# Kernel optimization log

Measured on AMD Instinct MI355X. Metric: run time of the kernel, lower is better.

The kernel has to match this reference:

```python
import jax, jax.numpy as jnp
import numpy as np

N_EMBD = 768
N_HEAD = 12
HEAD_DIM = N_EMBD // N_HEAD


def setup_inputs() -> dict:
    key = jax.random.key(0)
    k0, k1, k2, k3, k4 = jax.random.split(key, 5)
    B, T, C = 2, 4096, N_EMBD
    x = jax.random.normal(k0, (B, T, C), dtype=jnp.float32)
    # c_attn: Linear(C, 3C); c_proj: Linear(C, C). torch Linear: y = x @ W.T + b
    s = 1.0 / np.sqrt(C)
    W_attn = jax.random.uniform(k1, (3 * C, C), dtype=jnp.float32, minval=-s, maxval=s)
    b_attn = jax.random.uniform(k2, (3 * C,), dtype=jnp.float32, minval=-s, maxval=s)
    W_proj = jax.random.uniform(k3, (C, C), dtype=jnp.float32, minval=-s, maxval=s)
    b_proj = jax.random.uniform(k4, (C,), dtype=jnp.float32, minval=-s, maxval=s)
    return {"x": x, "W_attn": W_attn, "b_attn": b_attn, "W_proj": W_proj, "b_proj": b_proj}


def reference(x, W_attn, b_attn, W_proj, b_proj):
    B, T, C = x.shape
    H, D = N_HEAD, HEAD_DIM
    qkv = x @ W_attn.T + b_attn                      # [B,T,3C]
    q, k, v = jnp.split(qkv, 3, axis=-1)
    # [B,T,C] -> [B,H,T,D]
    q = q.reshape(B, T, H, D).transpose(0, 2, 1, 3)
    k = k.reshape(B, T, H, D).transpose(0, 2, 1, 3)
    v = v.reshape(B, T, H, D).transpose(0, 2, 1, 3)
    scale = 1.0 / jnp.sqrt(jnp.asarray(D, dtype=x.dtype))
    att = jnp.einsum('bhqd,bhkd->bhqk', q, k) * scale  # [B,H,T,T]
    att = jax.nn.softmax(att, axis=-1)
    y = jnp.einsum('bhqk,bhkd->bhqd', att, v)          # [B,H,T,D]
    y = y.transpose(0, 2, 1, 3).reshape(B, T, C)
    return y @ W_proj.T + b_proj
```

## Files before the change

### kernel.cpp

```cpp
#include <hip/hip_runtime.h>
#include <stdint.h>
#include <stddef.h>

typedef __bf16 bf16_t;
typedef bf16_t bf16x4 __attribute__((ext_vector_type(4)));
typedef bf16_t bf16x8 __attribute__((ext_vector_type(8)));
typedef float  f32x4  __attribute__((ext_vector_type(4)));
typedef _Float16 f16_t;
typedef f16_t f16x2 __attribute__((ext_vector_type(2)));
typedef f16_t f16x4 __attribute__((ext_vector_type(4)));
typedef f16_t f16x8 __attribute__((ext_vector_type(8)));
typedef __fp16 fp16x2_raw __attribute__((ext_vector_type(2)));

__device__ __forceinline__ f16x2 pkrtz(float a, float b) {
    fp16x2_raw r = __builtin_amdgcn_cvt_pkrtz(a, b);
    union { fp16x2_raw r; f16x2 h; } u;
    u.r = r;
    return u.h;
}

#define MFMA_BF16_K32(a, b, c) __builtin_amdgcn_mfma_f32_16x16x32_bf16(a, b, c, 0, 0, 0)
#define MFMA_F16_K32(a, b, c)  __builtin_amdgcn_mfma_f32_16x16x32_f16(a, b, c, 0, 0, 0)

#define SBAR()   __builtin_amdgcn_s_barrier()
#define SCHEDB() __builtin_amdgcn_sched_barrier(0)
#define WAITV(N) asm volatile("s_waitcnt vmcnt(" #N ")" ::: "memory")

__device__ __forceinline__ void gload_lds16(const void* g, void* l) {
    __builtin_amdgcn_global_load_lds(
        (const __attribute__((address_space(1))) void*)g,
        (__attribute__((address_space(3))) void*)l,
        16, 0, 0);
}

#define NX 1572864
#define NWA 442368
#define NWP 147456
__global__ void cvt_all(const float* __restrict__ x, const float* __restrict__ Wa,
                        const float* __restrict__ Wp, bf16_t* __restrict__ xb,
                        bf16_t* __restrict__ Wab, bf16_t* __restrict__ Wpb) {
    int i = blockIdx.x * blockDim.x + threadIdx.x;
    const float4* src; bf16_t* dst; int j;
    if (i < NX)            { src = (const float4*)x;  dst = xb;  j = i; }
    else if (i < NX + NWA) { src = (const float4*)Wa; dst = Wab; j = i - NX; }
    else                   { src = (const float4*)Wp; dst = Wpb; j = i - NX - NWA; }
    float4 f = src[j];
    bf16x4 o = { (bf16_t)f.x, (bf16_t)f.y, (bf16_t)f.z, (bf16_t)f.w };
    ((bf16x4*)dst)[j] = o;
}

template <int KDIM>
__device__ __forceinline__ void gemm_mainloop(
    const bf16_t* __restrict__ A, const bf16_t* __restrict__ Bt,
    bf16_t* As, bf16_t* Bs, int m0, int n0, int wave, int lane, f32x4 acc[4][4])
{
    const int quad = lane >> 4, l15 = lane & 15;
    const int wm = ((wave >> 1) << 6), wn = ((wave & 1) << 6);

    const int srow = (wave << 4) + (lane >> 2);
    const int sw   = (((lane & 3) ^ ((srow >> 1) & 3)) << 3);
    const bf16_t* gA = A  + (size_t)(m0 + srow) * KDIM + sw;
    const bf16_t* gB = Bt + (size_t)(n0 + srow) * KDIM + sw;
    const int loff = wave * 512;
    const int xorv = ((quad ^ ((l15 >> 1) & 3)) << 3);

    auto stage = [&](int k0, int buf) {
        bf16_t* a0 = As + buf * 4096 + loff;
        bf16_t* b0 = Bs + buf * 4096 + loff;
        gload_lds16(gA + k0,                     a0);
        gload_lds16(gA + (size_t)64 * KDIM + k0, a0 + 2048);
        gload_lds16(gB + k0,                     b0);
        gload_lds16(gB + (size_t)64 * KDIM + k0, b0 + 2048);
    };

    stage(0, 0);
    int buf = 0;
    for (int k0 = 0; k0 < KDIM; k0 += 32, buf ^= 1) {
        WAITV(0);
        __syncthreads();
        if (k0 + 32 < KDIM) stage(k0 + 32, buf ^ 1);
        const bf16_t* as = As + buf * 4096;
        const bf16_t* bs = Bs + buf * 4096;
        bf16x8 af[4], bfr[4];
#pragma unroll
        for (int t = 0; t < 4; t++) {
            af[t]  = *(const bf16x8*)(as + (wm + t * 16 + l15) * 32 + xorv);
            bfr[t] = *(const bf16x8*)(bs + (wn + t * 16 + l15) * 32 + xorv);
        }
#pragma unroll
        for (int mt = 0; mt < 4; mt++)
#pragma unroll
            for (int nt = 0; nt < 4; nt++)
                acc[mt][nt] = MFMA_BF16_K32(af[mt], bfr[nt], acc[mt][nt]);
    }
}

__global__ __launch_bounds__(256) void gemm_qkv(
    const bf16_t* __restrict__ A,
    const bf16_t* __restrict__ Bt,
    const float* __restrict__ bias,
    bf16_t* __restrict__ qo, bf16_t* __restrict__ ko, f16_t* __restrict__ vo)
{
    __shared__ bf16_t As[2 * 128 * 32];
    __shared__ bf16_t Bs[2 * 128 * 32];
    const int tid = threadIdx.x, wave = tid >> 6, lane = tid & 63;
    const int quad = lane >> 4, l15 = lane & 15;
    const int m0 = blockIdx.y * 128, n0 = blockIdx.x * 128;
    f32x4 acc[4][4] = {};
    gemm_mainloop<768>(A, Bt, As, Bs, m0, n0, wave, lane, acc);

    const int wm = ((wave >> 1) << 6), wn = ((wave & 1) << 6);
#pragma unroll
    for (int nt = 0; nt < 4; nt++) {
        const int cc = n0 + wn + nt * 16 + l15;
        const float bia = bias[cc];
        const int which = cc / 768;
        const int rem = cc - which * 768;
        const int h = rem >> 6, d = rem & 63;
        if (which < 2) {
            bf16_t* dst = (which == 0) ? qo : ko;
#pragma unroll
            for (int mt = 0; mt < 4; mt++) {
#pragma unroll
                for (int r = 0; r < 4; r++) {
                    const int row = m0 + wm + mt * 16 + quad * 4 + r;
                    const int b = row >> 12, t = row & 4095;
                    dst[((size_t)(b * 12 + h) * 4096 + t) * 64 + d] =
                        (bf16_t)(acc[mt][nt][r] + bia);
                }
            }
        } else {
#pragma unroll
            for (int mt = 0; mt < 4; mt++) {
                const int row0 = m0 + wm + mt * 16 + quad * 4;
                const int b = row0 >> 12, t0 = row0 & 4095;
                f16x4 ov = { (f16_t)(acc[mt][nt][0] + bia),
                             (f16_t)(acc[mt][nt][1] + bia),
                             (f16_t)(acc[mt][nt][2] + bia),
                             (f16_t)(acc[mt][nt][3] + bia) };
                *(f16x4*)(vo + ((size_t)(b * 12 + h) * 64 + d) * 4096 + t0) = ov;
            }
        }
    }
}

__global__ __launch_bounds__(256) void gemm_proj(
    const bf16_t* __restrict__ A,
    const bf16_t* __restrict__ Bt,
    const float* __restrict__ bias,
    float* __restrict__ out)
{
    __shared__ bf16_t As[2 * 128 * 32];
    __shared__ bf16_t Bs[2 * 128 * 32];
    const int tid = threadIdx.x, wave = tid >> 6, lane = tid & 63;
    const int quad = lane >> 4, l15 = lane & 15;
    const int m0 = blockIdx.y * 128, n0 = blockIdx.x * 128;
    f32x4 acc[4][4] = {};
    gemm_mainloop<768>(A, Bt, As, Bs, m0, n0, wave, lane, acc);

    const int wm = ((wave >> 1) << 6), wn = ((wave & 1) << 6);
#pragma unroll
    for (int nt = 0; nt < 4; nt++) {
        const int cc = n0 + wn + nt * 16 + l15;
        const float bia = bias[cc];
#pragma unroll
        for (int mt = 0; mt < 4; mt++) {
#pragma unroll
            for (int r = 0; r < 4; r++) {
                const int row = m0 + wm + mt * 16 + quad * 4 + r;
                out[(size_t)row * 768 + cc] = acc[mt][nt][r] + bia;
            }
        }
    }
}

#define QSCALE 0.1803368801f
__global__ __launch_bounds__(256, 3) void attn_fwd(
    const bf16_t* __restrict__ qg, const bf16_t* __restrict__ kg,
    const f16_t* __restrict__ vtg, bf16_t* __restrict__ y)
{
    __shared__ __align__(16) char smem[32768];
    bf16_t* Ks0 = (bf16_t*)(smem);
    bf16_t* Ks1 = (bf16_t*)(smem + 8192);
    f16_t*  Vt0 = (f16_t*)(smem + 16384);
    f16_t*  Vt1 = (f16_t*)(smem + 24576);
    float*  Red  = (float*)(smem);
    float*  Psr  = (float*)(smem + 17408);
    float*  PsT  = (float*)(smem + 18432);

    const int tid = threadIdx.x, wave = tid >> 6, lane = tid & 63;
    const int quad = lane >> 4, l15 = lane & 15;

    const int blk = blockIdx.x;
    const int xcd = blk & 7;
    const int idx = blk >> 3;
    const int hl  = idx % 3;
    const int qt  = idx / 3;
    const int bh  = xcd * 3 + hl;
    const int b = bh / 12, h = bh - b * 12;
    const size_t base = (size_t)bh * 4096 * 64;

    bf16x8 qf[4][2];
#pragma unroll
    for (int qc = 0; qc < 4; qc++) {
        const int qrow = qt * 64 + qc * 16 + l15;
        qf[qc][0] = *(const bf16x8*)(qg + base + (size_t)qrow * 64 + quad * 8);
        qf[qc][1] = *(const bf16x8*)(qg + base + (size_t)qrow * 64 + 32 + quad * 8);
#pragma unroll
        for (int j = 0; j < 8; j++) {
            qf[qc][0][j] = (bf16_t)((float)qf[qc][0][j] * QSCALE);
            qf[qc][1][j] = (bf16_t)((float)qf[qc][1][j] * QSCALE);
        }
    }

    f32x4 O[4][4] = {};
    f32x4 PS[4] = {};
    f16x8 ones8;
#pragma unroll
    for (int j = 0; j < 8; j++) ones8[j] = (f16_t)1.0f;

    const int srow8 = tid >> 3;
    const int sc8   = (tid & 7) ^ (srow8 & 7);
    const int l8 = l15 & 7;
    const int w16 = wave << 4;
    const int ksoff = (quad ^ l8) << 3;
    const int vslot = ((wave << 1) | (quad >> 1)) ^ l8;
    const int q0off = (quad & 1) * 8;

    auto stage_k = [&](const bf16_t* kp_, bf16_t* Kd) {
#pragma unroll
        for (int i = 0; i < 2; i++)
            gload_lds16(kp_ + (i * 32 + srow8) * 64 + sc8 * 8, Kd + (i * 256 + tid) * 8);
    };
    auto stage_v = [&](const f16_t* vp_, f16_t* Vd) {
#pragma unroll
        for (int i = 0; i < 2; i++)
            gload_lds16(vp_ + (size_t)(i * 32 + srow8) * 4096 + sc8 * 8, Vd + (i * 256 + tid) * 8);
    };

    const bf16_t* kp = kg + base;
    const f16_t*  vp = vtg + base;
    stage_k(kp, Ks0); stage_k(kp + 4096, Ks1);
    stage_v(vp, Vt0); stage_v(vp + 64, Vt1);
    __syncthreads();

    for (int p = 0; p < 32; p++) {
        const bf16_t* krA = Ks0 + (w16 + l15) * 64;
        const bf16_t* krB = Ks1 + (w16 + l15) * 64;
        bf16x8 kfA0 = *(const bf16x8*)(krA + ksoff);
        bf16x8 kfA1 = *(const bf16x8*)(krA + (ksoff ^ 32));
        bf16x8 kfB0 = *(const bf16x8*)(krB + ksoff);
        bf16x8 kfB1 = *(const bf16x8*)(krB + (ksoff ^ 32));
        f32x4 scA[4], scB[4];
        __builtin_amdgcn_s_setprio(1);
#pragma unroll
        for (int qc = 0; qc < 4; qc++) {
            f32x4 s = {};
            s = MFMA_BF16_K32(kfA0, qf[qc][0], s);
            s = MFMA_BF16_K32(kfA1, qf[qc][1], s);
            scA[qc] = s;
        }
#pragma unroll
        for (int qc = 0; qc < 4; qc++) {
            f32x4 s = {};
            s = MFMA_BF16_K32(kfB0, qf[qc][0], s);
            s = MFMA_BF16_K32(kfB1, qf[qc][1], s);
            scB[qc] = s;
        }
        __builtin_amdgcn_s_setprio(0);
        f16x8 pf8[4];
#pragma unroll
        for (int qc = 0; qc < 4; qc++) {
            float a0 = __builtin_amdgcn_exp2f(scA[qc][0]);
            float a1 = __builtin_amdgcn_exp2f(scA[qc][1]);
            float a2 = __builtin_amdgcn_exp2f(scA[qc][2]);
            float a3 = __builtin_amdgcn_exp2f(scA[qc][3]);
            float b0 = __builtin_amdgcn_exp2f(scB[qc][0]);
            float b1 = __builtin_amdgcn_exp2f(scB[qc][1]);
            float b2 = __builtin_amdgcn_exp2f(scB[qc][2]);
            float b3 = __builtin_amdgcn_exp2f(scB[qc][3]);
            f16x2 loA = pkrtz(a0, a1);
            f16x2 hiA = pkrtz(a2, a3);
            f16x2 loB = pkrtz(b0, b1);
            f16x2 hiB = pkrtz(b2, b3);
            union { f16x8 v; f16x2 h[4]; } u;
            u.h[0] = loA; u.h[1] = hiA; u.h[2] = loB; u.h[3] = hiB;
            pf8[qc] = u.v;
        }
        WAITV(0);
        SBAR();
        SCHEDB();
        if (p < 31) {
            const bf16_t* kn = kp + (size_t)(p + 1) * 8192;
            stage_k(kn, Ks0); stage_k(kn + 4096, Ks1);
        }
        __builtin_amdgcn_s_setprio(1);
#pragma unroll
        for (int dt = 0; dt < 4; dt++) {
            const char* vrA = (const char*)(Vt0 + (dt * 16 + l15) * 64);
            const char* vrB = (const char*)(Vt1 + (dt * 16 + l15) * 64);
            f16x4 vA = *(const f16x4*)(vrA + vslot * 16 + q0off);
            f16x4 vB = *(const f16x4*)(vrB + vslot * 16 + q0off);
            union { f16x8 v; f16x4 h[2]; } uv;
            uv.h[0] = vA; uv.h[1] = vB;
#pragma unroll
            for (int qc = 0; qc < 4; qc++)
                O[dt][qc] = MFMA_F16_K32(uv.v, pf8[qc], O[dt][qc]);
        }
#pragma unroll
        for (int qc = 0; qc < 4; qc++)
            PS[qc] = MFMA_F16_K32(ones8, pf8[qc], PS[qc]);
        __builtin_amdgcn_s_setprio(0);
        WAITV(0);
        SBAR();
        SCHEDB();
        if (p < 31) {
            const f16_t* vn = vp + (size_t)(p + 1) * 128;
            stage_v(vn, Vt0); stage_v(vn + 64, Vt1);
        }
    }

    __syncthreads();
    if (wave == 2) {
#pragma unroll
        for (int dt = 0; dt < 4; dt++)
#pragma unroll
            for (int qc = 0; qc < 4; qc++)
                *(f32x4*)(Red + (qc * 16 + l15) * 68 + dt * 16 + quad * 4) = O[dt][qc];
    }
    if (quad == 0) {
#pragma unroll
        for (int qc = 0; qc < 4; qc++) Psr[wave * 64 + qc * 16 + l15] = PS[qc][0];
    }
    __syncthreads();
    if (wave == 0) {
#pragma unroll
        for (int dt = 0; dt < 4; dt++)
#pragma unroll
            for (int qc = 0; qc < 4; qc++)
                O[dt][qc] += *(const f32x4*)(Red + (qc * 16 + l15) * 68 + dt * 16 + quad * 4);
    } else if (wave == 3) {
        PsT[lane] = Psr[lane] + Psr[64 + lane] + Psr[128 + lane] + Psr[192 + lane];
    }
    __syncthreads();
    if (wave == 3) {
#pragma unroll
        for (int dt = 0; dt < 4; dt++)
#pragma unroll
            for (int qc = 0; qc < 4; qc++)
                *(f32x4*)(Red + (qc * 16 + l15) * 68 + dt * 16 + quad * 4) = O[dt][qc];
    }
    __syncthreads();
    if (wave == 1) {
#pragma unroll
        for (int dt = 0; dt < 4; dt++)
#pragma unroll
            for (int qc = 0; qc < 4; qc++)
                O[dt][qc] += *(const f32x4*)(Red + (qc * 16 + l15) * 68 + dt * 16 + quad * 4);
    }
    __syncthreads();
    if (wave == 1) {
#pragma unroll
        for (int dt = 0; dt < 4; dt++)
#pragma unroll
            for (int qc = 0; qc < 4; qc++)
                *(f32x4*)(Red + (qc * 16 + l15) * 68 + dt * 16 + quad * 4) = O[dt][qc];
    }
    __syncthreads();
    if (wave == 0) {
#pragma unroll
        for (int qc = 0; qc < 4; qc++) {
            const float rcp = 1.0f / PsT[qc * 16 + l15];
            const int t = qt * 64 + qc * 16 + l15;
            bf16_t* yr = y + ((size_t)b * 4096 + t) * 768 + h * 64 + quad * 4;
#pragma unroll
            for (int dt = 0; dt < 4; dt++) {
                f32x4 o4 = O[dt][qc] +
                    *(const f32x4*)(Red + (qc * 16 + l15) * 68 + dt * 16 + quad * 4);
                bf16x4 ov = { (bf16_t)(o4[0] * rcp), (bf16_t)(o4[1] * rcp),
                              (bf16_t)(o4[2] * rcp), (bf16_t)(o4[3] * rcp) };
                *(bf16x4*)(yr + dt * 16) = ov;
            }
        }
    }
}

extern "C" void kernel_launch(void* const* d_in, const int* in_sizes, int n_in,
                              void* d_out, int out_size, void* d_ws, size_t ws_size,
                              hipStream_t stream) {
    const float* x  = (const float*)d_in[0];
    const float* Wa = (const float*)d_in[1];
    const float* ba = (const float*)d_in[2];
    const float* Wp = (const float*)d_in[3];
    const float* bp = (const float*)d_in[4];
    float* out = (float*)d_out;

    char* ws = (char*)d_ws;
    bf16_t* xb  = (bf16_t*)(ws);
    bf16_t* Wab = (bf16_t*)(ws + 12582912);
    bf16_t* Wpb = (bf16_t*)(ws + 16121856);
    bf16_t* qb  = (bf16_t*)(ws + 17301504);
    bf16_t* kb  = (bf16_t*)(ws + 29884416);
    f16_t*  vtb = (f16_t*)(ws + 42467328);
    bf16_t* yb  = (bf16_t*)(ws + 55050240);

    cvt_all<<<8448, 256, 0, stream>>>(x, Wa, Wp, xb, Wab, Wpb);
    gemm_qkv <<<dim3(18, 64), 256, 0, stream>>>(xb, Wab, ba, qb, kb, vtb);
    attn_fwd <<<1536, 256, 0, stream>>>(qb, kb, vtb, yb);
    gemm_proj<<<dim3( 6, 64), 256, 0, stream>>>(yb, Wpb, bp, out);
}
```

Measured before the change: 271.1 us.

## Block V^T into 8-token chunks and shrink projection GEMM tile to 64 rows

The QKV GEMM now writes V^T in a blocked layout where each 8-token chunk stores all 64 head dims contiguously. The attention kernel's V staging reads contiguous 1 KB rows instead of 4096-strided rows, which should give better global load coalescing. Separately, the projection GEMM moves to a 64x128 tile with a new mainloop, doubling the grid from 384 to 768 blocks so more CUs are busy. The trade-off is less operand reuse per block, and the LDS swizzle has to stay consistent with the new V addressing.

```diff
diff --git a/kernel.cpp b/kernel.cpp
--- a/kernel.cpp
+++ b/kernel.cpp
@@ -95,6 +95,52 @@
     }
 }
 
+template <int KDIM>
+__device__ __forceinline__ void gemm_mainloop64(
+    const bf16_t* __restrict__ A, const bf16_t* __restrict__ Bt,
+    bf16_t* As, bf16_t* Bs, int m0, int n0, int wave, int lane, f32x4 acc[4][2])
+{
+    const int quad = lane >> 4, l15 = lane & 15;
+    const int wn = wave << 5;
+
+    const int srow = (wave << 4) + (lane >> 2);
+    const int sw   = (((lane & 3) ^ ((srow >> 1) & 3)) << 3);
+    const bf16_t* gA = A  + (size_t)(m0 + srow) * KDIM + sw;
+    const bf16_t* gB = Bt + (size_t)(n0 + srow) * KDIM + sw;
+    const int loff = wave * 512;
+    const int xorv = ((quad ^ ((l15 >> 1) & 3)) << 3);
+
+    auto stage = [&](int k0, int buf) {
+        bf16_t* a0 = As + buf * 2048 + loff;
+        bf16_t* b0 = Bs + buf * 4096 + loff;
+        gload_lds16(gA + k0,                     a0);
+        gload_lds16(gB + k0,                     b0);
+        gload_lds16(gB + (size_t)64 * KDIM + k0, b0 + 2048);
+    };
+
+    stage(0, 0);
+    int buf = 0;
+    for (int k0 = 0; k0 < KDIM; k0 += 32, buf ^= 1) {
+        WAITV(0);
+        __syncthreads();
+        if (k0 + 32 < KDIM) stage(k0 + 32, buf ^ 1);
+        const bf16_t* as = As + buf * 2048;
+        const bf16_t* bs = Bs + buf * 4096;
+        bf16x8 af[4], bfr[2];
+#pragma unroll
+        for (int t = 0; t < 4; t++)
+            af[t]  = *(const bf16x8*)(as + (t * 16 + l15) * 32 + xorv);
+#pragma unroll
+        for (int t = 0; t < 2; t++)
+            bfr[t] = *(const bf16x8*)(bs + (wn + t * 16 + l15) * 32 + xorv);
+#pragma unroll
+        for (int mt = 0; mt < 4; mt++)
+#pragma unroll
+            for (int nt = 0; nt < 2; nt++)
+                acc[mt][nt] = MFMA_BF16_K32(af[mt], bfr[nt], acc[mt][nt]);
+    }
+}
+
 __global__ __launch_bounds__(256) void gemm_qkv(
     const bf16_t* __restrict__ A,
     const bf16_t* __restrict__ Bt,
@@ -138,7 +184,8 @@
                              (f16_t)(acc[mt][nt][1] + bia),
                              (f16_t)(acc[mt][nt][2] + bia),
                              (f16_t)(acc[mt][nt][3] + bia) };
-                *(f16x4*)(vo + ((size_t)(b * 12 + h) * 64 + d) * 4096 + t0) = ov;
+                *(f16x4*)(vo + ((size_t)(b * 12 + h) * 512 + (t0 >> 3)) * 512
+                             + (size_t)d * 8 + (t0 & 7)) = ov;
             }
         }
     }
@@ -150,24 +197,24 @@
     const float* __restrict__ bias,
     float* __restrict__ out)
 {
-    __shared__ bf16_t As[2 * 128 * 32];
+    __shared__ bf16_t As[2 * 64 * 32];
     __shared__ bf16_t Bs[2 * 128 * 32];
     const int tid = threadIdx.x, wave = tid >> 6, lane = tid & 63;
     const int quad = lane >> 4, l15 = lane & 15;
-    const int m0 = blockIdx.y * 128, n0 = blockIdx.x * 128;
-    f32x4 acc[4][4] = {};
-    gemm_mainloop<768>(A, Bt, As, Bs, m0, n0, wave, lane, acc);
-
-    const int wm = ((wave >> 1) << 6), wn = ((wave & 1) << 6);
-#pragma unroll
-    for (int nt = 0; nt < 4; nt++) {
+    const int m0 = blockIdx.y * 64, n0 = blockIdx.x * 128;
+    f32x4 acc[4][2] = {};
+    gemm_mainloop64<768>(A, Bt, As, Bs, m0, n0, wave, lane, acc);
+
+    const int wn = wave << 5;
+#pragma unroll
+    for (int nt = 0; nt < 2; nt++) {
         const int cc = n0 + wn + nt * 16 + l15;
         const float bia = bias[cc];
 #pragma unroll
         for (int mt = 0; mt < 4; mt++) {
 #pragma unroll
             for (int r = 0; r < 4; r++) {
-                const int row = m0 + wm + mt * 16 + quad * 4 + r;
+                const int row = m0 + mt * 16 + quad * 4 + r;
                 out[(size_t)row * 768 + cc] = acc[mt][nt][r] + bia;
             }
         }
@@ -232,16 +279,17 @@
         for (int i = 0; i < 2; i++)
             gload_lds16(kp_ + (i * 32 + srow8) * 64 + sc8 * 8, Kd + (i * 256 + tid) * 8);
     };
-    auto stage_v = [&](const f16_t* vp_, f16_t* Vd) {
+    const f16_t* vg = vtg + base;
+    auto stage_v = [&](int tb8, f16_t* Vd) {
 #pragma unroll
         for (int i = 0; i < 2; i++)
-            gload_lds16(vp_ + (size_t)(i * 32 + srow8) * 4096 + sc8 * 8, Vd + (i * 256 + tid) * 8);
+            gload_lds16(vg + (size_t)(tb8 + sc8) * 512 + (i * 32 + srow8) * 8,
+                        Vd + (i * 256 + tid) * 8);
     };
 
     const bf16_t* kp = kg + base;
-    const f16_t*  vp = vtg + base;
     stage_k(kp, Ks0); stage_k(kp + 4096, Ks1);
-    stage_v(vp, Vt0); stage_v(vp + 64, Vt1);
+    stage_v(0, Vt0); stage_v(8, Vt1);
     __syncthreads();
 
     for (int p = 0; p < 32; p++) {
@@ -315,8 +363,7 @@
         SBAR();
         SCHEDB();
         if (p < 31) {
-            const f16_t* vn = vp + (size_t)(p + 1) * 128;
-            stage_v(vn, Vt0); stage_v(vn + 64, Vt1);
+            stage_v((p + 1) * 16, Vt0); stage_v((p + 1) * 16 + 8, Vt1);
         }
     }
 
@@ -407,5 +454,5 @@
     cvt_all<<<8448, 256, 0, stream>>>(x, Wa, Wp, xb, Wab, Wpb);
     gemm_qkv <<<dim3(18, 64), 256, 0, stream>>>(xb, Wab, ba, qb, kb, vtb);
     attn_fwd <<<1536, 256, 0, stream>>>(qb, kb, vtb, yb);
-    gemm_proj<<<dim3( 6, 64), 256, 0, stream>>>(yb, Wpb, bp, out);
-}
+    gemm_proj<<<dim3(6, 128), 256, 0, stream>>>(yb, Wpb, bp, out);
+}
```

Result: slower. 297.8 us (+9.9%).
